# Optimization experiments

Hardware: AMD Instinct MI355X
Metric: run time of the kernel (lower is better)

The kernel has to match this reference:

```python
import jax, jax.numpy as jnp
import numpy as np

BSZ, SEQ, DK = 16, 2048, 64


def setup_inputs() -> dict:
    key = jax.random.key(0)
    kq, kk, kv, kp = jax.random.split(key, 4)
    Q = jax.random.normal(kq, (BSZ, SEQ, DK), dtype=jnp.float32)
    K = jax.random.normal(kk, (BSZ, SEQ, DK), dtype=jnp.float32)
    V = jax.random.normal(kv, (BSZ, SEQ, DK), dtype=jnp.float32)
    # learned relative-position key projection, Parameter(dk, sizeSeq)
    Krelpos = jax.random.normal(kp, (DK, SEQ), dtype=jnp.float32) * (1.0 / np.sqrt(DK))
    return {"Q": Q, "K": K, "V": V, "Krelpos": Krelpos}


def reference(Q, K, V, Krelpos):
    b, S, dk = Q.shape
    # content scores: [b, S, S]
    QK = jnp.einsum('bsd,btd->bst', Q, K)
    # relative-position bias via skew trick
    QP = jnp.einsum('bsd,dt->bst', Q, Krelpos)                     # [b, S, S]
    QP = jnp.concatenate([jnp.zeros((b, S, 1), QP.dtype), QP], axis=2)  # [b, S, S+1]
    QK = QK + QP.reshape(b, S + 1, S)[:, 1:, :]                    # skewed -> [b, S, S]
    # causal mask: -inf strictly above diagonal
    causal = jnp.tril(jnp.ones((S, S), dtype=bool))
    mask = jnp.where(causal, jnp.zeros((), QK.dtype), -jnp.inf)
    A = jax.nn.softmax(QK / jnp.sqrt(jnp.asarray(dk, QK.dtype)) + mask, axis=2)
    # dropout p=0.0 -> identity
    return jnp.einsum('bst,btd->bsd', A, V)
```

## Files before the change

### kernel.cpp

```cpp
#include <hip/hip_runtime.h>
#include <math.h>

#define BSZ 16
#define SEQ 2048
#define DKD 64
#define NTH 256

typedef __attribute__((ext_vector_type(8))) short bf16x8;
typedef __attribute__((ext_vector_type(8))) short short8;
typedef __attribute__((ext_vector_type(4))) float f32x4;

__device__ __forceinline__ short f2bf(float x) {
  union { float f; unsigned u; } c; c.f = x;
  unsigned r = c.u + 0x7fffu + ((c.u >> 16) & 1u);
  return (short)(r >> 16);
}

#define GLD16(gsrc, ldst)                                                                  \
  __builtin_amdgcn_global_load_lds((const __attribute__((address_space(1))) void*)(gsrc), \
                                   (__attribute__((address_space(3))) void*)(ldst), 16, 0, 0)

#define CH(row, c8) (((row) << 3) + ((c8) ^ ((row) & 7)))


__launch_bounds__(NTH)
__global__ void pre_convert(const float* __restrict__ K, const float* __restrict__ V,
                            const float* __restrict__ P, short* __restrict__ Kbf,
                            short* __restrict__ VTbf, short* __restrict__ PTbf) {
  __shared__ short T[64 * 65];
  const int blk = blockIdx.x;
  const int tid = threadIdx.x;
  if (blk < 1024) {
    const int b = blk >> 6, ch = blk & 63;
    const float* Kb = K + ((size_t)(b * SEQ + ch * 32)) * DKD;
    const float* Vb = V + ((size_t)(b * SEQ + ch * 32)) * DKD;
    const int r = tid >> 3, c8 = (tid & 7) << 3;
    float4 a0 = *(const float4*)(Kb + r * DKD + c8);
    float4 a1 = *(const float4*)(Kb + r * DKD + c8 + 4);
    short8 ko;
    ko[0] = f2bf(a0.x); ko[1] = f2bf(a0.y); ko[2] = f2bf(a0.z); ko[3] = f2bf(a0.w);
    ko[4] = f2bf(a1.x); ko[5] = f2bf(a1.y); ko[6] = f2bf(a1.z); ko[7] = f2bf(a1.w);
    *(short8*)(Kbf + ((size_t)(b * SEQ + ch * 32 + r)) * DKD + c8) = ko;
    float4 v0 = *(const float4*)(Vb + r * DKD + c8);
    float4 v1 = *(const float4*)(Vb + r * DKD + c8 + 4);
    T[(c8 + 0) * 33 + r] = f2bf(v0.x); T[(c8 + 1) * 33 + r] = f2bf(v0.y);
    T[(c8 + 2) * 33 + r] = f2bf(v0.z); T[(c8 + 3) * 33 + r] = f2bf(v0.w);
    T[(c8 + 4) * 33 + r] = f2bf(v1.x); T[(c8 + 5) * 33 + r] = f2bf(v1.y);
    T[(c8 + 6) * 33 + r] = f2bf(v1.z); T[(c8 + 7) * 33 + r] = f2bf(v1.w);
    __syncthreads();
    const int d = tid >> 2, q8 = (tid & 3) << 3;
    short8 w;
    #pragma unroll
    for (int j = 0; j < 8; ++j) w[j] = T[d * 33 + q8 + j];
    *(short8*)(VTbf + ((size_t)(b * DKD + d)) * SEQ + ch * 32 + q8) = w;
  } else if (blk < 1056) {
    const int c0 = (blk - 1024) * 64;
    const int d = tid >> 2, cc4 = (tid & 3) << 4;
    #pragma unroll
    for (int j4 = 0; j4 < 4; ++j4) {
      const int c = cc4 + j4 * 4;
      float4 pv = *(const float4*)(P + (size_t)d * SEQ + c0 + c);
      T[(c + 0) * 65 + d] = f2bf(pv.x);
      T[(c + 1) * 65 + d] = f2bf(pv.y);
      T[(c + 2) * 65 + d] = f2bf(pv.z);
      T[(c + 3) * 65 + d] = f2bf(pv.w);
    }
    __syncthreads();
    const int c = tid >> 2, d4 = (tid & 3) << 4;
    short8 w0, w1;
    #pragma unroll
    for (int j = 0; j < 8; ++j) { w0[j] = T[c * 65 + d4 + j]; w1[j] = T[c * 65 + d4 + 8 + j]; }
    short* Po = PTbf + ((size_t)(c0 + c)) * DKD + d4;
    *(short8*)(Po + 0) = w0;
    *(short8*)(Po + 8) = w1;
  } else {
    short8 z = {0, 0, 0, 0, 0, 0, 0, 0};
    short* Po = PTbf + (size_t)SEQ * DKD + tid * 16;
    *(short8*)(Po + 0) = z;
    *(short8*)(Po + 8) = z;
  }
}

__launch_bounds__(NTH, 4)
__global__ void attn_split(const float* __restrict__ Q,
                           const short* __restrict__ Kbf,
                           const short* __restrict__ VTbf,
                           const short* __restrict__ PTbf,
                           float* __restrict__ Oacc,
                           float* __restrict__ Lacc) {
  __shared__ __align__(16) short Ks[64 * 64];
  __shared__ __align__(16) short VsT[64 * 64];
  __shared__ __align__(16) short PsT[2 * 64 * 64];
  __shared__ __align__(16) short Pp[64 * 64];

  const int tid = threadIdx.x;
  const int lane = tid & 63;
  const int wave = tid >> 6;
  const int l16 = lane & 15;
  const int quad = lane >> 4;

  const int i = blockIdx.x;
  const int qidx = i >> 5;
  const int s = i & 31;
  const int b = s & 15;
  const int h = s >> 4;
  const int qt = (qidx < 16) ? (31 - qidx) : (qidx - 16);
  const int r0 = qt * 64;
  const int m = (qt + 2) >> 1;
  const int kt0 = h ? m : 0;
  const int kt1 = h ? (qt + 1) : m;
  const float SC = 0.125f * 1.4426950408889634f;

  bf16x8 aq[2];
  {
    const float* Qr = Q + ((size_t)(b * SEQ + r0 + wave * 16 + l16)) * DKD + quad * 8;
    #pragma unroll
    for (int ks = 0; ks < 2; ++ks) {
      float4 x = *(const float4*)(Qr + ks * 32);
      float4 y = *(const float4*)(Qr + ks * 32 + 4);
      bf16x8 t;
      t[0] = f2bf(x.x * SC); t[1] = f2bf(x.y * SC); t[2] = f2bf(x.z * SC); t[3] = f2bf(x.w * SC);
      t[4] = f2bf(y.x * SC); t[5] = f2bf(y.y * SC); t[6] = f2bf(y.z * SC); t[7] = f2bf(y.w * SC);
      aq[ks] = t;
    }
  }

  int gsrc[4];
  bool gcar[4];
  #pragma unroll
  for (int r = 0; r < 4; ++r) {
    int o = 15 - (quad * 4 + r);
    int ssrc = l16 + o;
    gsrc[r] = (quad << 4) | (ssrc & 15);
    gcar[r] = (ssrc >= 16);
  }

  bf16x8 ONES;
  #pragma unroll
  for (int j = 0; j < 8; ++j) ONES[j] = (short)0x3F80;

  f32x4 oacc[4];
  #pragma unroll
  for (int t = 0; t < 4; ++t)
    #pragma unroll
    for (int j = 0; j < 4; ++j) oacc[t][j] = 0.f;
  f32x4 bl;
  #pragma unroll
  for (int j = 0; j < 4; ++j) bl[j] = 0.f;

  const int Blo0 = 31 - qt;

  for (int kt = kt0; kt < kt1; ++kt) {
    const int j0 = kt * 64;
    __syncthreads();

    #pragma unroll
    for (int half = 0; half < 2; ++half) {
      const int ii = wave * 2 + half;
      const int j = ii * 64 + lane;
      {
        const int k = j >> 3, c8 = (j & 7) ^ (k & 7);
        GLD16(Kbf + ((size_t)(b * SEQ + j0 + k)) * DKD + c8 * 8, Ks + ii * 512);
      }
      {
        const int d = j >> 3, c8 = (j & 7) ^ (d & 7);
        GLD16(VTbf + ((size_t)(b * DKD + d)) * SEQ + j0 + c8 * 8, VsT + ii * 512);
      }
    }
    {
      const int Bg = Blo0 + kt + 1;
      #pragma unroll
      for (int half = 0; half < 2; ++half) {
        const int ii = wave * 2 + half;
        const int j = ii * 64 + lane;
        const int c = j >> 3, c8 = (j & 7) ^ (c & 7);
        GLD16(PTbf + ((size_t)(Bg * 64 + c)) * DKD + c8 * 8,
              PsT + ((Bg & 1) << 12) + ii * 512);
      }
      if (kt == kt0) {
        const int Bl = Blo0 + kt0;
        #pragma unroll
        for (int half = 0; half < 2; ++half) {
          const int ii = wave * 2 + half;
          const int j = ii * 64 + lane;
          const int c = j >> 3, c8 = (j & 7) ^ (c & 7);
          GLD16(PTbf + ((size_t)(Bl * 64 + c)) * DKD + c8 * 8,
                PsT + ((Bl & 1) << 12) + ii * 512);
        }
      }
    }
    __syncthreads();

    f32x4 sacc[4];
    #pragma unroll
    for (int t = 0; t < 4; ++t)
      #pragma unroll
      for (int j = 0; j < 4; ++j) sacc[t][j] = 0.f;
    #pragma unroll
    for (int ks = 0; ks < 2; ++ks)
      #pragma unroll
      for (int t = 0; t < 4; ++t) {
        bf16x8 bk = *(const bf16x8*)&Ks[CH(t * 16 + l16, ks * 4 + quad) << 3];
        sacc[t] = __builtin_amdgcn_mfma_f32_16x16x32_bf16(aq[ks], bk, sacc[t], 0, 0, 0);
      }

    f32x4 bacc[5];
    #pragma unroll
    for (int t = 0; t < 5; ++t)
      #pragma unroll
      for (int j = 0; j < 4; ++j) bacc[t][j] = 0.f;
    #pragma unroll
    for (int tt = 0; tt < 5; ++tt) {
      const int c = (tt + 3 - wave) * 16 + l16;
      const int pan = (Blo0 + kt + (c >> 6)) & 1;
      const int pr = c & 63;
      #pragma unroll
      for (int ks = 0; ks < 2; ++ks) {
        bf16x8 bp = *(const bf16x8*)&PsT[(pan << 12) + (CH(pr, ks * 4 + quad) << 3)];
        bacc[tt] = __builtin_amdgcn_mfma_f32_16x16x32_bf16(aq[ks], bp, bacc[tt], 0, 0, 0);
      }
    }

    float g[5][4];
    #pragma unroll
    for (int tt = 0; tt < 5; ++tt)
      #pragma unroll
      for (int r = 0; r < 4; ++r) g[tt][r] = __shfl(bacc[tt][r], gsrc[r], 64);

    const bool diag = (kt == qt);
    #pragma unroll
    for (int r = 0; r < 4; ++r) {
      const int rs = quad * 4 + r;
      #pragma unroll
      for (int t = 0; t < 4; ++t) {
        float sc = sacc[t][r] + (gcar[r] ? g[t + 1][r] : g[t][r]);
        if (diag && (t * 16 + l16 > wave * 16 + rs)) sc = -INFINITY;
        float e = exp2f(sc);
        const int row = wave * 16 + rs;
        Pp[(CH(row, t * 2 + (l16 >> 3)) << 3) + (l16 & 7)] = f2bf(e);
      }
    }

    #pragma unroll
    for (int ks = 0; ks < 2; ++ks) {
      bf16x8 ap = *(const bf16x8*)&Pp[CH(wave * 16 + l16, ks * 4 + quad) << 3];
      #pragma unroll
      for (int dt = 0; dt < 4; ++dt) {
        bf16x8 bv = *(const bf16x8*)&VsT[CH(dt * 16 + l16, ks * 4 + quad) << 3];
        oacc[dt] = __builtin_amdgcn_mfma_f32_16x16x32_bf16(ap, bv, oacc[dt], 0, 0, 0);
      }
      bl = __builtin_amdgcn_mfma_f32_16x16x32_bf16(ap, ONES, bl, 0, 0, 0);
    }
  }

  if (kt1 > kt0) {
    float* Ob = Oacc + ((size_t)(b * SEQ + r0)) * DKD;
    #pragma unroll
    for (int r = 0; r < 4; ++r) {
      const int row = wave * 16 + quad * 4 + r;
      #pragma unroll
      for (int dt = 0; dt < 4; ++dt)
        unsafeAtomicAdd(&Ob[(size_t)row * DKD + dt * 16 + l16], oacc[dt][r]);
    }
    if (l16 == 0) {
      #pragma unroll
      for (int r = 0; r < 4; ++r)
        unsafeAtomicAdd(&Lacc[b * SEQ + r0 + wave * 16 + quad * 4 + r], bl[r]);
    }
  }
}

__launch_bounds__(NTH)
__global__ void norm_out(float* __restrict__ O, const float* __restrict__ L) {
  const int tid = threadIdx.x;
  const int row = blockIdx.x * 16 + (tid >> 4);
  const int c4 = (tid & 15) << 2;
  const float rl = 1.0f / L[row];
  float4* p = (float4*)(O + (size_t)row * DKD + c4);
  float4 v = *p;
  v.x *= rl; v.y *= rl; v.z *= rl; v.w *= rl;
  *p = v;
}

extern "C" void kernel_launch(void* const* d_in, const int* in_sizes, int n_in,
                              void* d_out, int out_size, void* d_ws, size_t ws_size,
                              hipStream_t stream) {
  const float* Q = (const float*)d_in[0];
  const float* K = (const float*)d_in[1];
  const float* V = (const float*)d_in[2];
  const float* P = (const float*)d_in[3];
  float* O = (float*)d_out;

  short* Kbf = (short*)d_ws;
  short* VTbf = (short*)((char*)d_ws + 4194304);
  short* PTbf = (short*)((char*)d_ws + 8388608);
  float* Lacc = (float*)((char*)d_ws + 8658944);

  hipMemsetAsync(O, 0, (size_t)BSZ * SEQ * DKD * sizeof(float), stream);
  hipMemsetAsync(Lacc, 0, (size_t)BSZ * SEQ * sizeof(float), stream);
  hipLaunchKernelGGL(pre_convert, dim3(1057), dim3(NTH), 0, stream, K, V, P, Kbf, VTbf, PTbf);
  hipLaunchKernelGGL(attn_split, dim3(1024), dim3(NTH), 0, stream, Q, Kbf, VTbf, PTbf, O, Lacc);
  hipLaunchKernelGGL(norm_out, dim3(BSZ * SEQ / 16), dim3(NTH), 0, stream, O, Lacc);
}
```

Measured before the change: 140.3 us.

## Keep P in registers via MFMA transpose, fold memsets into pre-convert

The P tile no longer takes a trip through shared memory. The exp values are packed to bf16 in registers and transposed with MFMAs against selector matrices, then fed as the B operand of a transposed O^T = V^T P^T product, with V read in a matching layout. This drops the Pp LDS buffer and its store/load round trip. The output atomics now go through an LDS transpose so each thread adds contiguous row segments. The two hipMemsetAsync calls are replaced by extra zeroing blocks in pre_convert, which removes two separate operations. The cost is more MFMA issue, split ushort4 LDS reads, and an extra barrier at the epilogue.

```diff
diff --git a/kernel.cpp b/kernel.cpp
--- a/kernel.cpp
+++ b/kernel.cpp
@@ -16,6 +16,10 @@
   return (short)(r >> 16);
 }
 
+__device__ __forceinline__ int pkbf(float hi, float lo) {
+  return (int)__builtin_amdgcn_perm(__float_as_uint(hi), __float_as_uint(lo), 0x07060302u);
+}
+
 #define GLD16(gsrc, ldst)                                                                  \
   __builtin_amdgcn_global_load_lds((const __attribute__((address_space(1))) void*)(gsrc), \
                                    (__attribute__((address_space(3))) void*)(ldst), 16, 0, 0)
@@ -26,7 +30,8 @@
 __launch_bounds__(NTH)
 __global__ void pre_convert(const float* __restrict__ K, const float* __restrict__ V,
                             const float* __restrict__ P, short* __restrict__ Kbf,
-                            short* __restrict__ VTbf, short* __restrict__ PTbf) {
+                            short* __restrict__ VTbf, short* __restrict__ PTbf,
+                            float* __restrict__ Ozero, float* __restrict__ Lzero) {
   __shared__ short T[64 * 65];
   const int blk = blockIdx.x;
   const int tid = threadIdx.x;
@@ -73,11 +78,21 @@
     short* Po = PTbf + ((size_t)(c0 + c)) * DKD + d4;
     *(short8*)(Po + 0) = w0;
     *(short8*)(Po + 8) = w1;
-  } else {
+  } else if (blk == 1056) {
     short8 z = {0, 0, 0, 0, 0, 0, 0, 0};
     short* Po = PTbf + (size_t)SEQ * DKD + tid * 16;
     *(short8*)(Po + 0) = z;
     *(short8*)(Po + 8) = z;
+  } else if (blk < 1569) {
+    const int u = blk - 1057;
+    float4 z = {0.f, 0.f, 0.f, 0.f};
+    float4* p = (float4*)(Ozero + (size_t)u * 4096 + tid * 16);
+    p[0] = z; p[1] = z; p[2] = z; p[3] = z;
+  } else {
+    const int u = blk - 1569;
+    float4 z = {0.f, 0.f, 0.f, 0.f};
+    float4* p = (float4*)(Lzero + (size_t)u * 4096 + tid * 16);
+    p[0] = z; p[1] = z; p[2] = z; p[3] = z;
   }
 }
 
@@ -88,10 +103,10 @@
                            const short* __restrict__ PTbf,
                            float* __restrict__ Oacc,
                            float* __restrict__ Lacc) {
-  __shared__ __align__(16) short Ks[64 * 64];
-  __shared__ __align__(16) short VsT[64 * 64];
-  __shared__ __align__(16) short PsT[2 * 64 * 64];
-  __shared__ __align__(16) short Pp[64 * 64];
+  __shared__ __align__(16) short smem[16384];
+  short* Ks  = smem;
+  short* VsT = smem + 4096;
+  short* PsT = smem + 8192;
 
   const int tid = threadIdx.x;
   const int lane = tid & 63;
@@ -130,14 +145,22 @@
   #pragma unroll
   for (int r = 0; r < 4; ++r) {
     int o = 15 - (quad * 4 + r);
-    int ssrc = l16 + o;
-    gsrc[r] = (quad << 4) | (ssrc & 15);
-    gcar[r] = (ssrc >= 16);
-  }
-
-  bf16x8 ONES;
-  #pragma unroll
-  for (int j = 0; j < 8; ++j) ONES[j] = (short)0x3F80;
+    int ss = l16 + o;
+    gsrc[r] = (quad << 4) | (ss & 15);
+    gcar[r] = (ss >= 16);
+  }
+
+  union i4v { int4 i; bf16x8 v; };
+  i4v ONESu; ONESu.i = make_int4(0x3F803F80, 0x3F803F80, 0x3F803F80, 0x3F803F80);
+  i4v S0u, S1u;
+  S0u.i = make_int4(0, 0, 0, 0);
+  S1u.i = make_int4(0, 0, 0, 0);
+  if (quad == (l16 >> 2)) {
+    const int j = l16 & 3;
+    const int val = 0x3F80 << ((j & 1) * 16);
+    if (j < 2) { S0u.i.x = val; S1u.i.z = val; }
+    else       { S0u.i.y = val; S1u.i.w = val; }
+  }
 
   f32x4 oacc[4];
   #pragma unroll
@@ -204,69 +227,89 @@
         sacc[t] = __builtin_amdgcn_mfma_f32_16x16x32_bf16(aq[ks], bk, sacc[t], 0, 0, 0);
       }
 
-    f32x4 bacc[5];
-    #pragma unroll
-    for (int t = 0; t < 5; ++t)
-      #pragma unroll
-      for (int j = 0; j < 4; ++j) bacc[t][j] = 0.f;
+    float g[5][4];
     #pragma unroll
     for (int tt = 0; tt < 5; ++tt) {
+      f32x4 bacc;
+      #pragma unroll
+      for (int j = 0; j < 4; ++j) bacc[j] = 0.f;
       const int c = (tt + 3 - wave) * 16 + l16;
       const int pan = (Blo0 + kt + (c >> 6)) & 1;
       const int pr = c & 63;
       #pragma unroll
       for (int ks = 0; ks < 2; ++ks) {
         bf16x8 bp = *(const bf16x8*)&PsT[(pan << 12) + (CH(pr, ks * 4 + quad) << 3)];
-        bacc[tt] = __builtin_amdgcn_mfma_f32_16x16x32_bf16(aq[ks], bp, bacc[tt], 0, 0, 0);
-      }
-    }
-
-    float g[5][4];
-    #pragma unroll
-    for (int tt = 0; tt < 5; ++tt)
-      #pragma unroll
-      for (int r = 0; r < 4; ++r) g[tt][r] = __shfl(bacc[tt][r], gsrc[r], 64);
+        bacc = __builtin_amdgcn_mfma_f32_16x16x32_bf16(aq[ks], bp, bacc, 0, 0, 0);
+      }
+      #pragma unroll
+      for (int r = 0; r < 4; ++r) g[tt][r] = __shfl(bacc[r], gsrc[r], 64);
+    }
 
     const bool diag = (kt == qt);
-    #pragma unroll
-    for (int r = 0; r < 4; ++r) {
-      const int rs = quad * 4 + r;
-      #pragma unroll
-      for (int t = 0; t < 4; ++t) {
+    float e[4][4];
+    #pragma unroll
+    for (int t = 0; t < 4; ++t)
+      #pragma unroll
+      for (int r = 0; r < 4; ++r) {
         float sc = sacc[t][r] + (gcar[r] ? g[t + 1][r] : g[t][r]);
-        if (diag && (t * 16 + l16 > wave * 16 + rs)) sc = -INFINITY;
-        float e = exp2f(sc);
-        const int row = wave * 16 + rs;
-        Pp[(CH(row, t * 2 + (l16 >> 3)) << 3) + (l16 & 7)] = f2bf(e);
-      }
-    }
-
-    #pragma unroll
-    for (int ks = 0; ks < 2; ++ks) {
-      bf16x8 ap = *(const bf16x8*)&Pp[CH(wave * 16 + l16, ks * 4 + quad) << 3];
+        if (diag && (t * 16 + l16 > wave * 16 + quad * 4 + r)) sc = -INFINITY;
+        e[t][r] = exp2f(sc);
+      }
+
+    i4v ap0, ap1;
+    ap0.i.x = pkbf(e[0][1], e[0][0]); ap0.i.y = pkbf(e[0][3], e[0][2]);
+    ap0.i.z = pkbf(e[1][1], e[1][0]); ap0.i.w = pkbf(e[1][3], e[1][2]);
+    ap1.i.x = pkbf(e[2][1], e[2][0]); ap1.i.y = pkbf(e[2][3], e[2][2]);
+    ap1.i.z = pkbf(e[3][1], e[3][0]); ap1.i.w = pkbf(e[3][3], e[3][2]);
+
+    f32x4 zero4;
+    #pragma unroll
+    for (int j = 0; j < 4; ++j) zero4[j] = 0.f;
+    f32x4 Dt[4];
+    Dt[0] = __builtin_amdgcn_mfma_f32_16x16x32_bf16(ap0.v, S0u.v, zero4, 0, 0, 0);
+    Dt[1] = __builtin_amdgcn_mfma_f32_16x16x32_bf16(ap0.v, S1u.v, zero4, 0, 0, 0);
+    Dt[2] = __builtin_amdgcn_mfma_f32_16x16x32_bf16(ap1.v, S0u.v, zero4, 0, 0, 0);
+    Dt[3] = __builtin_amdgcn_mfma_f32_16x16x32_bf16(ap1.v, S1u.v, zero4, 0, 0, 0);
+
+    i4v bp0, bp1;
+    bp0.i.x = pkbf(Dt[0][1], Dt[0][0]); bp0.i.y = pkbf(Dt[0][3], Dt[0][2]);
+    bp0.i.z = pkbf(Dt[1][1], Dt[1][0]); bp0.i.w = pkbf(Dt[1][3], Dt[1][2]);
+    bp1.i.x = pkbf(Dt[2][1], Dt[2][0]); bp1.i.y = pkbf(Dt[2][3], Dt[2][2]);
+    bp1.i.z = pkbf(Dt[3][1], Dt[3][0]); bp1.i.w = pkbf(Dt[3][3], Dt[3][2]);
+
+    #pragma unroll
+    for (int tp = 0; tp < 2; ++tp) {
+      const bf16x8 bpk = tp ? bp1.v : bp0.v;
+      bl = __builtin_amdgcn_mfma_f32_16x16x32_bf16(ONESu.v, bpk, bl, 0, 0, 0);
       #pragma unroll
       for (int dt = 0; dt < 4; ++dt) {
-        bf16x8 bv = *(const bf16x8*)&VsT[CH(dt * 16 + l16, ks * 4 + quad) << 3];
-        oacc[dt] = __builtin_amdgcn_mfma_f32_16x16x32_bf16(ap, bv, oacc[dt], 0, 0, 0);
-      }
-      bl = __builtin_amdgcn_mfma_f32_16x16x32_bf16(ap, ONES, bl, 0, 0, 0);
-    }
-  }
-
-  if (kt1 > kt0) {
-    float* Ob = Oacc + ((size_t)(b * SEQ + r0)) * DKD;
-    #pragma unroll
-    for (int r = 0; r < 4; ++r) {
-      const int row = wave * 16 + quad * 4 + r;
-      #pragma unroll
-      for (int dt = 0; dt < 4; ++dt)
-        unsafeAtomicAdd(&Ob[(size_t)row * DKD + dt * 16 + l16], oacc[dt][r]);
-    }
-    if (l16 == 0) {
-      #pragma unroll
-      for (int r = 0; r < 4; ++r)
-        unsafeAtomicAdd(&Lacc[b * SEQ + r0 + wave * 16 + quad * 4 + r], bl[r]);
-    }
+        const int row = dt * 16 + l16;
+        ushort4 lo = *(const ushort4*)&VsT[(CH(row, tp * 4 + (quad >> 1)) << 3) + (quad & 1) * 4];
+        ushort4 hi = *(const ushort4*)&VsT[(CH(row, tp * 4 + 2 + (quad >> 1)) << 3) + (quad & 1) * 4];
+        bf16x8 av;
+        av[0] = (short)lo.x; av[1] = (short)lo.y; av[2] = (short)lo.z; av[3] = (short)lo.w;
+        av[4] = (short)hi.x; av[5] = (short)hi.y; av[6] = (short)hi.z; av[7] = (short)hi.w;
+        oacc[dt] = __builtin_amdgcn_mfma_f32_16x16x32_bf16(av, bpk, oacc[dt], 0, 0, 0);
+      }
+    }
+  }
+
+  __syncthreads();
+  float* Te = (float*)smem;
+  #pragma unroll
+  for (int dt = 0; dt < 4; ++dt)
+    #pragma unroll
+    for (int r = 0; r < 4; ++r)
+      Te[(wave * 16 + l16) * 65 + dt * 16 + quad * 4 + r] = oacc[dt][r];
+  __syncthreads();
+  {
+    const int q = tid >> 2, cg0 = (tid & 3) * 16;
+    float* Ob = Oacc + ((size_t)(b * SEQ + r0 + q)) * DKD + cg0;
+    const float* Tr = Te + q * 65 + cg0;
+    #pragma unroll
+    for (int j = 0; j < 16; ++j) unsafeAtomicAdd(&Ob[j], Tr[j]);
+    if (quad == 0)
+      unsafeAtomicAdd(&Lacc[b * SEQ + r0 + wave * 16 + l16], bl[0]);
   }
 }
 
@@ -296,9 +339,9 @@
   short* PTbf = (short*)((char*)d_ws + 8388608);
   float* Lacc = (float*)((char*)d_ws + 8658944);
 
-  hipMemsetAsync(O, 0, (size_t)BSZ * SEQ * DKD * sizeof(float), stream);
-  hipMemsetAsync(Lacc, 0, (size_t)BSZ * SEQ * sizeof(float), stream);
-  hipLaunchKernelGGL(pre_convert, dim3(1057), dim3(NTH), 0, stream, K, V, P, Kbf, VTbf, PTbf);
-  hipLaunchKernelGGL(attn_split, dim3(1024), dim3(NTH), 0, stream, Q, Kbf, VTbf, PTbf, O, Lacc);
+  hipLaunchKernelGGL(pre_convert, dim3(1577), dim3(NTH), 0, stream,
+                     K, V, P, Kbf, VTbf, PTbf, O, Lacc);
+  hipLaunchKernelGGL(attn_split, dim3(1024), dim3(NTH), 0, stream,
+                     Q, Kbf, VTbf, PTbf, O, Lacc);
   hipLaunchKernelGGL(norm_out, dim3(BSZ * SEQ / 16), dim3(NTH), 0, stream, O, Lacc);
 }
```

Result: slower. 288.3 us (+105.4%).
